# Optimization experiments

Measured on AMD Instinct MI355X. Metric: run time of the kernel, lower is better.

Reference implementation:

```python
import jax, jax.numpy as jnp
import numpy as np

KINEMATIC_CHAIN = [[0,2,5,8,11],[0,1,4,7,10],[0,3,6,9,12,15],[9,14,17,19,21],[9,13,16,18,20]]
_paths = [c[1:] for c in KINEMATIC_CHAIN]
SEG_S = np.array([p[i] for p in _paths for i in range(len(p)-1)])      # [16] segment start joints
SEG_E = np.array([p[i+1] for p in _paths for i in range(len(p)-1)])    # [16] segment end joints
PATH_ID = np.array([k for k, p in enumerate(_paths) for _ in range(len(p)-1)])
N_PATHS = len(_paths)
P_ONEHOT = (PATH_ID[:, None] == np.arange(N_PATHS)[None, :]).astype(np.float32)  # [16,5]


def _safe_normalize(v):
    ss = jnp.sum(v * v, axis=-1, keepdims=True)
    return jnp.where(ss > 0, v / jnp.sqrt(jnp.where(ss > 0, ss, 1.0)), 0.0)


def _gli_pairwise(s1, e1, s2, e2):
    # all inputs broadcast to [..., 3]; returns Gauss linking integral per segment pair
    r13, r14 = s2 - s1, e2 - s1
    r23, r24 = s2 - e1, e2 - e1
    r12, r34 = e1 - s1, e2 - s2
    f0 = _safe_normalize(jnp.cross(r13, r14))
    f1 = _safe_normalize(jnp.cross(r14, r24))
    f2 = _safe_normalize(jnp.cross(r24, r23))
    f3 = _safe_normalize(jnp.cross(r23, r13))
    def asin_dot(a, b):
        return jnp.arcsin(jnp.clip(jnp.sum(a * b, -1), -1.0, 1.0))
    total = asin_dot(f0, f1) + asin_dot(f1, f2) + asin_dot(f2, f3) + asin_dot(f3, f0)
    sign = jnp.sum(jnp.cross(r34, r12) * r13, -1)
    mult = jnp.where(sign <= 0, -1.0, 1.0)
    return mult * total / (4.0 * jnp.pi)


def _bbox_xz(m):
    x, z = m[..., 0], m[..., 2]
    return x.min(-1), x.max(-1), z.min(-1), z.max(-1)


def setup_inputs() -> dict:
    key = jax.random.key(0)
    k1, k2 = jax.random.split(key)
    B, F, J = 64, 240, 22
    motion1 = jax.random.normal(k1, (B, F, J, 3), dtype=jnp.float32)
    motion2 = jax.random.normal(k2, (B, F, J, 3), dtype=jnp.float32)
    return {"motion1": motion1, "motion2": motion2}


def reference(motion1, motion2):
    B, F = motion1.shape[0], motion1.shape[1]
    P = jnp.asarray(P_ONEHOT, motion1.dtype)
    # gather all 16 skeleton segments, broadcast to 16x16 segment pairs
    s1 = motion1[..., SEG_S, :][..., :, None, :]   # [B,F,16,1,3]
    e1 = motion1[..., SEG_E, :][..., :, None, :]
    s2 = motion2[..., SEG_S, :][..., None, :, :]   # [B,F,1,16,3]
    e2 = motion2[..., SEG_E, :][..., None, :, :]
    gli_seg = _gli_pairwise(s1, e1, s2, e2)        # [B,F,16,16]
    # sum segment-pair GLIs into path-pair blocks -> [B,F,5,5]
    gli_pose = jnp.einsum('bfmn,mi,nj->bfij', gli_seg, P, P)

    # xz bounding-box overlap per frame, then dilate by 1 frame (window start-1..end+1)
    nx1, xx1, nz1, xz1 = _bbox_xz(motion1)
    nx2, xx2, nz2, xz2 = _bbox_xz(motion2)
    flag = (xx1 >= nx2) & (xx2 >= nx1) & (xz1 >= nz2) & (xz2 >= nz1)   # [B,F]
    pad = jnp.zeros_like(flag[:, :1])
    mask = flag | jnp.concatenate([flag[:, 1:], pad], 1) | jnp.concatenate([pad, flag[:, :-1]], 1)
    gli_motion = gli_pose * mask[..., None, None].astype(gli_pose.dtype)

    vel = jnp.abs(gli_motion[:, 1:] - gli_motion[:, :-1]).reshape(B, F - 1, -1)
    return vel.max(-1)
```

## Files before the change

### kernel.cpp

```cpp
#include <hip/hip_runtime.h>
#include <math.h>

#define BB 64
#define FF 240
#define NJ 22
#define NFRM (BB * FF)

#define PK8(a0,a1,a2,a3,a4,a5,a6,a7) \
  (  (unsigned long long)(a0)        | ((unsigned long long)(a1) << 5)  \
   | ((unsigned long long)(a2) << 10)| ((unsigned long long)(a3) << 15) \
   | ((unsigned long long)(a4) << 20)| ((unsigned long long)(a5) << 25) \
   | ((unsigned long long)(a6) << 30)| ((unsigned long long)(a7) << 35) )
static constexpr unsigned long long SEG_S_LO = PK8(2,5,8,1,4,7,3,6);
static constexpr unsigned long long SEG_S_HI = PK8(9,12,14,17,19,13,16,18);
static constexpr unsigned long long SEG_E_LO = PK8(5,8,11,4,7,10,6,9);
static constexpr unsigned long long SEG_E_HI = PK8(12,15,17,19,21,16,18,20);
static constexpr unsigned PO_PK = 0u | (3u<<5) | (6u<<10) | (10u<<15) | (13u<<20);
static constexpr unsigned PC_PK = 3u | (3u<<5) | (4u<<10) | (3u<<15)  | (3u<<20);

struct F3 { float x, y, z; };
__device__ __forceinline__ F3 sub(F3 a, F3 b){ return {a.x-b.x, a.y-b.y, a.z-b.z}; }
__device__ __forceinline__ F3 crs(F3 a, F3 b){
    return {fmaf(a.y, b.z, -a.z*b.y), fmaf(a.z, b.x, -a.x*b.z), fmaf(a.x, b.y, -a.y*b.x)};
}
__device__ __forceinline__ float dt(F3 a, F3 b){ return fmaf(a.x, b.x, fmaf(a.y, b.y, a.z*b.z)); }
__device__ __forceinline__ float clamp1(float d){ return fminf(fmaxf(d, -1.0f), 1.0f); }

__device__ __forceinline__ float asin_fast(float d){
    float ax = fabsf(d);
    float p = fmaf(fmaf(fmaf(-0.0187293f, ax, 0.0742610f), ax, -0.2121144f), ax, 1.5707288f);
    float r = 1.57079632679f - sqrtf(1.0f - ax) * p;
    return copysignf(r, d);
}

__global__ void __launch_bounds__(256) k_gli(const float* __restrict__ m1,
                                             const float* __restrict__ m2,
                                             float* __restrict__ gp,
                                             int* __restrict__ flags){
    __shared__ __align__(16) float pts[2][4][66];
    __shared__ __align__(16) float seg[4][2][16][12];
    __shared__ float g[4][256];
    int tid = threadIdx.x;
    int frame0 = blockIdx.x * 4;

    if (tid < 132){
        bool first = tid < 66;
        int u = first ? tid : tid - 66;
        const float4* src = first ? (const float4*)(m1 + (size_t)frame0 * 66)
                                  : (const float4*)(m2 + (size_t)frame0 * 66);
        ((float4*)pts)[(first ? 0 : 66) + u] = src[u];
    }
    __syncthreads();

    if (tid < 128){
        int m = tid & 15, mot = (tid >> 4) & 1, w0 = tid >> 5;
        unsigned long long ps = (m < 8) ? SEG_S_LO : SEG_S_HI;
        unsigned long long pe = (m < 8) ? SEG_E_LO : SEG_E_HI;
        int sh = (m & 7) * 5;
        int js = (int)((ps >> sh) & 31);
        int je = (int)((pe >> sh) & 31);
        const float* P = pts[mot][w0];
        float* dst = &seg[w0][mot][m][0];
        float4 a = {P[js*3], P[js*3+1], P[js*3+2], P[je*3]};
        float2 b = {P[je*3+1], P[je*3+2]};
        *(float4*)dst = a;
        *(float2*)(dst + 4) = b;
    }
    __syncthreads();

    int w = tid >> 6, lane = tid & 63;
    int n = lane & 15, q = lane >> 4;

    float4 sa = *(const float4*)&seg[w][1][n][0];
    float2 sb = *(const float2*)&seg[w][1][n][4];
    F3 s2 = {sa.x, sa.y, sa.z};
    F3 e2 = {sa.w, sb.x, sb.y};

    float rd01[4], rd12[4], rd23[4], rd30[4];
    float q01[4], q12[4], q23[4], q30[4];
    float sg[4];
    #pragma unroll
    for (int k = 0; k < 4; ++k){
        int m = q + 4 * k;
        float4 ta = *(const float4*)&seg[w][0][m][0];
        float2 tb = *(const float2*)&seg[w][0][m][4];
        F3 s1 = {ta.x, ta.y, ta.z};
        F3 e1 = {ta.w, tb.x, tb.y};
        F3 r13 = sub(s2, s1), r14 = sub(e2, s1);
        F3 r23 = sub(s2, e1), r24 = sub(e2, e1);
        F3 f0 = crs(r13, r14);
        F3 f1 = crs(r14, r24);
        F3 f2 = crs(r24, r23);
        F3 f3 = crs(r23, r13);
        float ss0 = dt(f0,f0), ss1 = dt(f1,f1), ss2 = dt(f2,f2), ss3 = dt(f3,f3);
        rd01[k] = dt(f0,f1); rd12[k] = dt(f1,f2);
        rd23[k] = dt(f2,f3); rd30[k] = dt(f3,f0);
        q01[k] = ss0*ss1; q12[k] = ss1*ss2; q23[k] = ss2*ss3; q30[k] = ss3*ss0;
        sg[k] = dt(f3, r14);
    }

    float i01[4], i12[4], i23[4], i30[4];
    #pragma unroll
    for (int k = 0; k < 4; ++k){
        i01[k] = rsqrtf(fmaxf(q01[k], 1e-30f));
        i12[k] = rsqrtf(fmaxf(q12[k], 1e-30f));
        i23[k] = rsqrtf(fmaxf(q23[k], 1e-30f));
        i30[k] = rsqrtf(fmaxf(q30[k], 1e-30f));
    }

    #pragma unroll
    for (int k = 0; k < 4; ++k){
        float t = asin_fast(clamp1(rd01[k] * i01[k]))
                + asin_fast(clamp1(rd12[k] * i12[k]))
                + asin_fast(clamp1(rd23[k] * i23[k]))
                + asin_fast(clamp1(rd30[k] * i30[k]));
        float r = (sg[k] >= 0.0f ? -t : t) * 0.07957747154594767f;
        int m = q + 4 * k;
        g[w][m * 16 + n] = r;
    }
    __syncthreads();

    if (tid < 100){
        int w2 = tid / 25, pp = tid - w2 * 25;
        int i = pp / 5, j = pp - i * 5;
        int poi = (int)((PO_PK >> (i*5)) & 31), pci = (int)((PC_PK >> (i*5)) & 31);
        int poj = (int)((PO_PK >> (j*5)) & 31), pcj = (int)((PC_PK >> (j*5)) & 31);
        float s = 0.0f;
        for (int a = 0; a < pci; ++a)
            for (int b = 0; b < pcj; ++b)
                s += g[w2][(poi + a) * 16 + (poj + b)];
        int fr = frame0 + w2;
        int bb = fr / FF, f = fr - bb * FF;
        gp[((size_t)bb * 25 + pp) * FF + f] = s;
    }
    else if (tid >= 128 && tid < 132){
        int w2 = tid - 128;
        const float* Q1 = pts[0][w2];
        const float* Q2 = pts[1][w2];
        float nx1 = 1e30f, xx1 = -1e30f, nz1 = 1e30f, xz1 = -1e30f;
        float nx2 = 1e30f, xx2 = -1e30f, nz2 = 1e30f, xz2 = -1e30f;
        #pragma unroll
        for (int j = 0; j < NJ; ++j){
            float x1 = Q1[j*3+0], z1 = Q1[j*3+2];
            nx1 = fminf(nx1, x1); xx1 = fmaxf(xx1, x1);
            nz1 = fminf(nz1, z1); xz1 = fmaxf(xz1, z1);
            float x2 = Q2[j*3+0], z2 = Q2[j*3+2];
            nx2 = fminf(nx2, x2); xx2 = fmaxf(xx2, x2);
            nz2 = fminf(nz2, z2); xz2 = fmaxf(xz2, z2);
        }
        flags[frame0 + w2] =
            (xx1 >= nx2 && xx2 >= nx1 && xz1 >= nz2 && xz2 >= nz1) ? 1 : 0;
    }
}

__global__ void __launch_bounds__(256) k_vel(const float* __restrict__ gp,
                                             const int* __restrict__ flags,
                                             float* __restrict__ out){
    int b = blockIdx.x;
    int f = threadIdx.x;
    if (f >= FF - 1) return;
    const int* fl = flags + b * FF;

    int v0 = fl[f] | fl[f + 1];
    if (f > 0) v0 |= fl[f - 1];
    float mk0 = v0 ? 1.0f : 0.0f;

    int v1 = fl[f] | fl[f + 1];
    if (f + 2 < FF) v1 |= fl[f + 2];
    float mk1 = v1 ? 1.0f : 0.0f;

    const float* gb = gp + (size_t)b * 25 * FF + f;
    float mx = 0.0f;
    #pragma unroll
    for (int p = 0; p < 25; ++p){
        float g0 = gb[p * FF];
        float g1 = gb[p * FF + 1];
        float d = fabsf(g1 * mk1 - g0 * mk0);
        mx = fmaxf(mx, d);
    }
    out[b * (FF - 1) + f] = mx;
}

extern "C" void kernel_launch(void* const* d_in, const int* in_sizes, int n_in,
                              void* d_out, int out_size, void* d_ws, size_t ws_size,
                              hipStream_t stream) {
    const float* m1 = (const float*)d_in[0];
    const float* m2 = (const float*)d_in[1];
    float* gp    = (float*)d_ws;
    int*   flags = (int*)((char*)d_ws + (size_t)BB * 25 * FF * 4);
    float* out = (float*)d_out;

    k_gli<<<NFRM / 4, 256, 0, stream>>>(m1, m2, gp, flags);
    k_vel<<<BB, 256, 0, stream>>>(gp, flags, out);
}
```

Before: 80.97 us.

## Process one frame per block with one segment pair per thread

```diff
diff --git a/kernel.cpp b/kernel.cpp
--- a/kernel.cpp
+++ b/kernel.cpp
@@ -33,59 +33,63 @@
     return copysignf(r, d);
 }
 
-__global__ void __launch_bounds__(256) k_gli(const float* __restrict__ m1,
-                                             const float* __restrict__ m2,
-                                             float* __restrict__ gp,
-                                             int* __restrict__ flags){
-    __shared__ __align__(16) float pts[2][4][66];
-    __shared__ __align__(16) float seg[4][2][16][12];
-    __shared__ float g[4][256];
+__global__ void __launch_bounds__(256) k_main(const float* __restrict__ m1,
+                                              const float* __restrict__ m2,
+                                              float* __restrict__ gp,
+                                              int* __restrict__ flags){
+    __shared__ __align__(8)  float pts[132];
+    __shared__ __align__(16) float seg[2][16][12];
+    __shared__ float g[256];
+    __shared__ float h[80];
+    __shared__ float ext[2][4];
     int tid = threadIdx.x;
-    int frame0 = blockIdx.x * 4;
+    int fr = blockIdx.x;
 
-    if (tid < 132){
-        bool first = tid < 66;
-        int u = first ? tid : tid - 66;
-        const float4* src = first ? (const float4*)(m1 + (size_t)frame0 * 66)
-                                  : (const float4*)(m2 + (size_t)frame0 * 66);
-        ((float4*)pts)[(first ? 0 : 66) + u] = src[u];
+    if (tid < 66){
+        bool first = tid < 33;
+        int u = first ? tid : tid - 33;
+        const float2* src = first ? (const float2*)(m1 + (size_t)fr * 66)
+                                  : (const float2*)(m2 + (size_t)fr * 66);
+        ((float2*)pts)[(first ? 0 : 33) + u] = src[u];
     }
     __syncthreads();
 
-    if (tid < 128){
-        int m = tid & 15, mot = (tid >> 4) & 1, w0 = tid >> 5;
+    if (tid < 32){
+        int m = tid & 15, mot = tid >> 4;
         unsigned long long ps = (m < 8) ? SEG_S_LO : SEG_S_HI;
         unsigned long long pe = (m < 8) ? SEG_E_LO : SEG_E_HI;
         int sh = (m & 7) * 5;
         int js = (int)((ps >> sh) & 31);
         int je = (int)((pe >> sh) & 31);
-        const float* P = pts[mot][w0];
-        float* dst = &seg[w0][mot][m][0];
-        float4 a = {P[js*3], P[js*3+1], P[js*3+2], P[je*3]};
-        float2 b = {P[je*3+1], P[je*3+2]};
-        *(float4*)dst = a;
-        *(float2*)(dst + 4) = b;
+        const float* P = pts + mot * 66;
+        float* d = &seg[mot][m][0];
+        d[0] = P[js*3]; d[1] = P[js*3+1]; d[2] = P[js*3+2];
+        d[3] = P[je*3]; d[4] = P[je*3+1]; d[5] = P[je*3+2];
+    } else if (tid < 34){
+        int mot = tid - 32;
+        const float* P = pts + mot * 66;
+        float nx = 1e30f, xx = -1e30f, nz = 1e30f, xz = -1e30f;
+        #pragma unroll
+        for (int j = 0; j < NJ; ++j){
+            float x = P[j*3], z = P[j*3+2];
+            nx = fminf(nx, x); xx = fmaxf(xx, x);
+            nz = fminf(nz, z); xz = fmaxf(xz, z);
+        }
+        ext[mot][0] = nx; ext[mot][1] = xx; ext[mot][2] = nz; ext[mot][3] = xz;
     }
     __syncthreads();
 
-    int w = tid >> 6, lane = tid & 63;
-    int n = lane & 15, q = lane >> 4;
-
-    float4 sa = *(const float4*)&seg[w][1][n][0];
-    float2 sb = *(const float2*)&seg[w][1][n][4];
-    F3 s2 = {sa.x, sa.y, sa.z};
-    F3 e2 = {sa.w, sb.x, sb.y};
-
-    float rd01[4], rd12[4], rd23[4], rd30[4];
-    float q01[4], q12[4], q23[4], q30[4];
-    float sg[4];
-    #pragma unroll
-    for (int k = 0; k < 4; ++k){
-        int m = q + 4 * k;
-        float4 ta = *(const float4*)&seg[w][0][m][0];
-        float2 tb = *(const float2*)&seg[w][0][m][4];
+    {
+        int n = tid & 15, m = tid >> 4;
+        float4 sa = *(const float4*)&seg[1][n][0];
+        float2 sb = *(const float2*)&seg[1][n][4];
+        F3 s2 = {sa.x, sa.y, sa.z};
+        F3 e2 = {sa.w, sb.x, sb.y};
+        float4 ta = *(const float4*)&seg[0][m][0];
+        float2 tb = *(const float2*)&seg[0][m][4];
         F3 s1 = {ta.x, ta.y, ta.z};
         F3 e1 = {ta.w, tb.x, tb.y};
+
         F3 r13 = sub(s2, s1), r14 = sub(e2, s1);
         F3 r23 = sub(s2, e1), r24 = sub(e2, e1);
         F3 f0 = crs(r13, r14);
@@ -93,63 +97,38 @@
         F3 f2 = crs(r24, r23);
         F3 f3 = crs(r23, r13);
         float ss0 = dt(f0,f0), ss1 = dt(f1,f1), ss2 = dt(f2,f2), ss3 = dt(f3,f3);
-        rd01[k] = dt(f0,f1); rd12[k] = dt(f1,f2);
-        rd23[k] = dt(f2,f3); rd30[k] = dt(f3,f0);
-        q01[k] = ss0*ss1; q12[k] = ss1*ss2; q23[k] = ss2*ss3; q30[k] = ss3*ss0;
-        sg[k] = dt(f3, r14);
-    }
-
-    float i01[4], i12[4], i23[4], i30[4];
-    #pragma unroll
-    for (int k = 0; k < 4; ++k){
-        i01[k] = rsqrtf(fmaxf(q01[k], 1e-30f));
-        i12[k] = rsqrtf(fmaxf(q12[k], 1e-30f));
-        i23[k] = rsqrtf(fmaxf(q23[k], 1e-30f));
-        i30[k] = rsqrtf(fmaxf(q30[k], 1e-30f));
-    }
-
-    #pragma unroll
-    for (int k = 0; k < 4; ++k){
-        float t = asin_fast(clamp1(rd01[k] * i01[k]))
-                + asin_fast(clamp1(rd12[k] * i12[k]))
-                + asin_fast(clamp1(rd23[k] * i23[k]))
-                + asin_fast(clamp1(rd30[k] * i30[k]));
-        float r = (sg[k] >= 0.0f ? -t : t) * 0.07957747154594767f;
-        int m = q + 4 * k;
-        g[w][m * 16 + n] = r;
+        float i01 = rsqrtf(fmaxf(ss0*ss1, 1e-30f));
+        float i12 = rsqrtf(fmaxf(ss1*ss2, 1e-30f));
+        float i23 = rsqrtf(fmaxf(ss2*ss3, 1e-30f));
+        float i30 = rsqrtf(fmaxf(ss3*ss0, 1e-30f));
+        float t = asin_fast(clamp1(dt(f0,f1) * i01))
+                + asin_fast(clamp1(dt(f1,f2) * i12))
+                + asin_fast(clamp1(dt(f2,f3) * i23))
+                + asin_fast(clamp1(dt(f3,f0) * i30));
+        float sg = dt(f3, r14);
+        g[tid] = (sg >= 0.0f ? -t : t) * 0.07957747154594767f;
     }
     __syncthreads();
 
-    if (tid < 100){
-        int w2 = tid / 25, pp = tid - w2 * 25;
-        int i = pp / 5, j = pp - i * 5;
+    if (tid < 80){
+        int i = tid >> 4, n = tid & 15;
         int poi = (int)((PO_PK >> (i*5)) & 31), pci = (int)((PC_PK >> (i*5)) & 31);
+        float s = 0.0f;
+        for (int a = 0; a < pci; ++a) s += g[(poi + a) * 16 + n];
+        h[i * 16 + n] = s;
+    } else if (tid == 80){
+        flags[fr] = (ext[0][1] >= ext[1][0] && ext[1][1] >= ext[0][0] &&
+                     ext[0][3] >= ext[1][2] && ext[1][3] >= ext[0][2]) ? 1 : 0;
+    }
+    __syncthreads();
+
+    if (tid < 25){
+        int i = tid / 5, j = tid - i * 5;
         int poj = (int)((PO_PK >> (j*5)) & 31), pcj = (int)((PC_PK >> (j*5)) & 31);
         float s = 0.0f;
-        for (int a = 0; a < pci; ++a)
-            for (int b = 0; b < pcj; ++b)
-                s += g[w2][(poi + a) * 16 + (poj + b)];
-        int fr = frame0 + w2;
+        for (int b = 0; b < pcj; ++b) s += h[i * 16 + poj + b];
         int bb = fr / FF, f = fr - bb * FF;
-        gp[((size_t)bb * 25 + pp) * FF + f] = s;
-    }
-    else if (tid >= 128 && tid < 132){
-        int w2 = tid - 128;
-        const float* Q1 = pts[0][w2];
-        const float* Q2 = pts[1][w2];
-        float nx1 = 1e30f, xx1 = -1e30f, nz1 = 1e30f, xz1 = -1e30f;
-        float nx2 = 1e30f, xx2 = -1e30f, nz2 = 1e30f, xz2 = -1e30f;
-        #pragma unroll
-        for (int j = 0; j < NJ; ++j){
-            float x1 = Q1[j*3+0], z1 = Q1[j*3+2];
-            nx1 = fminf(nx1, x1); xx1 = fmaxf(xx1, x1);
-            nz1 = fminf(nz1, z1); xz1 = fmaxf(xz1, z1);
-            float x2 = Q2[j*3+0], z2 = Q2[j*3+2];
-            nx2 = fminf(nx2, x2); xx2 = fmaxf(xx2, x2);
-            nz2 = fminf(nz2, z2); xz2 = fmaxf(xz2, z2);
-        }
-        flags[frame0 + w2] =
-            (xx1 >= nx2 && xx2 >= nx1 && xz1 >= nz2 && xz2 >= nz1) ? 1 : 0;
+        gp[((size_t)bb * 25 + tid) * FF + f] = s;
     }
 }
 
@@ -190,6 +169,6 @@
     int*   flags = (int*)((char*)d_ws + (size_t)BB * 25 * FF * 4);
     float* out = (float*)d_out;
 
-    k_gli<<<NFRM / 4, 256, 0, stream>>>(m1, m2, gp, flags);
+    k_main<<<NFRM, 256, 0, stream>>>(m1, m2, gp, flags);
     k_vel<<<BB, 256, 0, stream>>>(gp, flags, out);
 }
```

After: 86.79 us. 1.07x slower.

## Process one frame per 64-thread block and parallelize bbox reduction across lanes

Applied to the files above, without the earlier changes.

```diff
diff --git a/kernel.cpp b/kernel.cpp
--- a/kernel.cpp
+++ b/kernel.cpp
@@ -33,46 +33,53 @@
     return copysignf(r, d);
 }
 
-__global__ void __launch_bounds__(256) k_gli(const float* __restrict__ m1,
-                                             const float* __restrict__ m2,
-                                             float* __restrict__ gp,
-                                             int* __restrict__ flags){
-    __shared__ __align__(16) float pts[2][4][66];
-    __shared__ __align__(16) float seg[4][2][16][12];
-    __shared__ float g[4][256];
-    int tid = threadIdx.x;
-    int frame0 = blockIdx.x * 4;
+__global__ void __launch_bounds__(64, 4) k_main(const float* __restrict__ m1,
+                                                const float* __restrict__ m2,
+                                                float* __restrict__ gp,
+                                                int* __restrict__ flags){
+    __shared__ __align__(16) float pts[2][68];
+    __shared__ __align__(16) float seg[2][16][12];
+    __shared__ float g[256];
+    __shared__ float ext[8];
+    int lane = threadIdx.x;
+    int fr = blockIdx.x;
 
-    if (tid < 132){
-        bool first = tid < 66;
-        int u = first ? tid : tid - 66;
-        const float4* src = first ? (const float4*)(m1 + (size_t)frame0 * 66)
-                                  : (const float4*)(m2 + (size_t)frame0 * 66);
-        ((float4*)pts)[(first ? 0 : 66) + u] = src[u];
-    }
+    const float2* gsrc1 = (const float2*)(m1 + (size_t)fr * 66);
+    const float2* gsrc2 = (const float2*)(m2 + (size_t)fr * 66);
+    if (lane < 33) ((float2*)pts[0])[lane] = gsrc1[lane];
+    if (lane >= 31){ int u = lane - 31; if (u < 33) ((float2*)pts[1])[u] = gsrc2[u]; }
     __syncthreads();
 
-    if (tid < 128){
-        int m = tid & 15, mot = (tid >> 4) & 1, w0 = tid >> 5;
+    if (lane < 32){
+        int m = lane & 15, mot = lane >> 4;
         unsigned long long ps = (m < 8) ? SEG_S_LO : SEG_S_HI;
         unsigned long long pe = (m < 8) ? SEG_E_LO : SEG_E_HI;
         int sh = (m & 7) * 5;
         int js = (int)((ps >> sh) & 31);
         int je = (int)((pe >> sh) & 31);
-        const float* P = pts[mot][w0];
-        float* dst = &seg[w0][mot][m][0];
-        float4 a = {P[js*3], P[js*3+1], P[js*3+2], P[je*3]};
-        float2 b = {P[je*3+1], P[je*3+2]};
-        *(float4*)dst = a;
-        *(float2*)(dst + 4) = b;
+        const float* P = pts[mot];
+        float* d = &seg[mot][m][0];
+        d[0] = P[js*3]; d[1] = P[js*3+1]; d[2] = P[js*3+2];
+        d[3] = P[je*3]; d[4] = P[je*3+1]; d[5] = P[je*3+2];
+    } else if (lane < 40){
+        int sel = lane - 32;
+        int mot = sel >> 2;
+        int c = sel & 2;
+        bool mx = sel & 1;
+        const float* P = pts[mot];
+        float a = 1e30f;
+        #pragma unroll
+        for (int j = 0; j < NJ; ++j){
+            float v = P[j*3 + c];
+            a = fminf(a, mx ? -v : v);
+        }
+        ext[sel] = mx ? -a : a;
     }
     __syncthreads();
 
-    int w = tid >> 6, lane = tid & 63;
     int n = lane & 15, q = lane >> 4;
-
-    float4 sa = *(const float4*)&seg[w][1][n][0];
-    float2 sb = *(const float2*)&seg[w][1][n][4];
+    float4 sa = *(const float4*)&seg[1][n][0];
+    float2 sb = *(const float2*)&seg[1][n][4];
     F3 s2 = {sa.x, sa.y, sa.z};
     F3 e2 = {sa.w, sb.x, sb.y};
 
@@ -82,8 +89,8 @@
     #pragma unroll
     for (int k = 0; k < 4; ++k){
         int m = q + 4 * k;
-        float4 ta = *(const float4*)&seg[w][0][m][0];
-        float2 tb = *(const float2*)&seg[w][0][m][4];
+        float4 ta = *(const float4*)&seg[0][m][0];
+        float2 tb = *(const float2*)&seg[0][m][4];
         F3 s1 = {ta.x, ta.y, ta.z};
         F3 e1 = {ta.w, tb.x, tb.y};
         F3 r13 = sub(s2, s1), r14 = sub(e2, s1);
@@ -98,7 +105,6 @@
         q01[k] = ss0*ss1; q12[k] = ss1*ss2; q23[k] = ss2*ss3; q30[k] = ss3*ss0;
         sg[k] = dt(f3, r14);
     }
-
     float i01[4], i12[4], i23[4], i30[4];
     #pragma unroll
     for (int k = 0; k < 4; ++k){
@@ -107,7 +113,6 @@
         i23[k] = rsqrtf(fmaxf(q23[k], 1e-30f));
         i30[k] = rsqrtf(fmaxf(q30[k], 1e-30f));
     }
-
     #pragma unroll
     for (int k = 0; k < 4; ++k){
         float t = asin_fast(clamp1(rd01[k] * i01[k]))
@@ -115,41 +120,23 @@
                 + asin_fast(clamp1(rd23[k] * i23[k]))
                 + asin_fast(clamp1(rd30[k] * i30[k]));
         float r = (sg[k] >= 0.0f ? -t : t) * 0.07957747154594767f;
-        int m = q + 4 * k;
-        g[w][m * 16 + n] = r;
+        g[(q + 4*k) * 16 + n] = r;
     }
     __syncthreads();
 
-    if (tid < 100){
-        int w2 = tid / 25, pp = tid - w2 * 25;
-        int i = pp / 5, j = pp - i * 5;
+    if (lane < 25){
+        int i = lane / 5, j = lane - i * 5;
         int poi = (int)((PO_PK >> (i*5)) & 31), pci = (int)((PC_PK >> (i*5)) & 31);
         int poj = (int)((PO_PK >> (j*5)) & 31), pcj = (int)((PC_PK >> (j*5)) & 31);
         float s = 0.0f;
         for (int a = 0; a < pci; ++a)
             for (int b = 0; b < pcj; ++b)
-                s += g[w2][(poi + a) * 16 + (poj + b)];
-        int fr = frame0 + w2;
+                s += g[(poi + a) * 16 + (poj + b)];
         int bb = fr / FF, f = fr - bb * FF;
-        gp[((size_t)bb * 25 + pp) * FF + f] = s;
-    }
-    else if (tid >= 128 && tid < 132){
-        int w2 = tid - 128;
-        const float* Q1 = pts[0][w2];
-        const float* Q2 = pts[1][w2];
-        float nx1 = 1e30f, xx1 = -1e30f, nz1 = 1e30f, xz1 = -1e30f;
-        float nx2 = 1e30f, xx2 = -1e30f, nz2 = 1e30f, xz2 = -1e30f;
-        #pragma unroll
-        for (int j = 0; j < NJ; ++j){
-            float x1 = Q1[j*3+0], z1 = Q1[j*3+2];
-            nx1 = fminf(nx1, x1); xx1 = fmaxf(xx1, x1);
-            nz1 = fminf(nz1, z1); xz1 = fmaxf(xz1, z1);
-            float x2 = Q2[j*3+0], z2 = Q2[j*3+2];
-            nx2 = fminf(nx2, x2); xx2 = fmaxf(xx2, x2);
-            nz2 = fminf(nz2, z2); xz2 = fmaxf(xz2, z2);
-        }
-        flags[frame0 + w2] =
-            (xx1 >= nx2 && xx2 >= nx1 && xz1 >= nz2 && xz2 >= nz1) ? 1 : 0;
+        gp[((size_t)bb * 25 + lane) * FF + f] = s;
+    } else if (lane == 25){
+        flags[fr] = (ext[1] >= ext[4] && ext[5] >= ext[0] &&
+                     ext[3] >= ext[6] && ext[7] >= ext[2]) ? 1 : 0;
     }
 }
 
@@ -190,6 +177,6 @@
     int*   flags = (int*)((char*)d_ws + (size_t)BB * 25 * FF * 4);
     float* out = (float*)d_out;
 
-    k_gli<<<NFRM / 4, 256, 0, stream>>>(m1, m2, gp, flags);
+    k_main<<<NFRM, 64, 0, stream>>>(m1, m2, gp, flags);
     k_vel<<<BB, 256, 0, stream>>>(gp, flags, out);
 }
```

After: 83.11 us. 1.03x slower.
